# Kernel tuning notes

Measured on AMD Instinct MI355X. Metric: run time of the kernel, lower is better.

## Reference

```python
import jax, jax.numpy as jnp
import numpy as np
from itertools import combinations

H_RANK_MAX = 2
TP_RANK_MAX = 2
BASIS_RANK_MAX = 2
DIM = 3
N_NODES = 50000
N_EDGES = 400000
N_CHANNELS = 16
R_CUT = 10.0  # radial cutoff for Bessel RBF (assumed)


def find_combinations(a_max, b_max, s):
    if s > a_max + b_max or s < 0:
        return []
    return [(a, s - a) for a in range(max(0, s - b_max), min(a_max, s) + 1)]


def contraction_is_valid(n_in, n_out):
    # legs are removed in pairs (Kronecker-delta contractions)
    return (n_in >= n_out) and ((n_in - n_out) % 2 == 0)


def _matchings(legs):
    # all perfect matchings of an even-size list of leg indices
    if not legs:
        yield []
        return
    a = legs[0]
    for i in range(1, len(legs)):
        rest = legs[1:i] + legs[i + 1:]
        for m in _matchings(rest):
            yield [(a, legs[i])] + m


def contraction_specs(a, b, c_out):
    # all einsum strings contracting an [E,K,dim^a] x [E,K,dim^b] tensor product
    # (a+b legs total) down to c_out free Cartesian legs, pairing the rest.
    n = a + b
    specs = []
    for free in combinations(range(n), c_out):
        paired = [i for i in range(n) if i not in free]
        for m in _matchings(paired):
            lbl = {}
            it = iter('mnopqrstuvwxyz')
            for f in free:
                lbl[f] = next(it)
            for (i, j) in m:
                L = next(it)
                lbl[i] = L
                lbl[j] = L
            sa = ''.join(lbl[i] for i in range(a))
            sb = ''.join(lbl[i] for i in range(a, n))
            so = ''.join(lbl[f] for f in free)
            specs.append(f'ek{sa},ek{sb}->ek{so}')
    return specs


def e_rbf(r, n):
    # Bessel radial basis: n is [K,1], r is [E] -> [K,E]
    return jnp.sqrt(2.0 / R_CUT) * jnp.sin(n * jnp.pi * r / R_CUT) / r


def tensor_prod(r, order):
    # repeated outer product of unit vectors: order 0 -> [E], order k -> [E] + [DIM]*k
    out = jnp.ones(r.shape[0], dtype=r.dtype)
    for _ in range(order):
        out = jnp.einsum('e...,ed->e...d', out, r)
    return out


def setup_inputs() -> dict:
    key = jax.random.key(0)
    ks = jax.random.split(key, 7)
    h0 = jax.random.normal(ks[0], (N_NODES, N_CHANNELS), jnp.float32)
    h1 = jax.random.normal(ks[1], (N_NODES, N_CHANNELS, DIM), jnp.float32)
    h2 = jax.random.normal(ks[2], (N_NODES, N_CHANNELS, DIM, DIM), jnp.float32)
    pos = jax.random.normal(ks[3], (N_NODES, DIM), jnp.float32)
    channel_weights = jax.random.normal(ks[4], (H_RANK_MAX + 1, N_CHANNELS, N_CHANNELS), jnp.float32)
    src = jax.random.randint(ks[5], (N_EDGES,), 0, N_NODES, dtype=jnp.int32)
    off = jax.random.randint(ks[6], (N_EDGES,), 1, N_NODES, dtype=jnp.int32)
    dst = (src + off) % N_NODES  # no self-loops -> no zero distances
    edge_index = jnp.stack([src, dst])
    return {"h0": h0, "h1": h1, "h2": h2, "pos": pos,
            "channel_weights": channel_weights, "edge_index": edge_index}


def reference(h0, h1, h2, pos, channel_weights, edge_index):
    h = [h0, h1, h2]
    src, dst = edge_index[0], edge_index[1]
    rel = pos[src] - pos[dst]                       # [E,3]
    dists = jnp.linalg.norm(rel, axis=-1)           # [E]
    unit = rel / dists[:, None]
    hg = [g[dst] for g in h]                        # per-edge gathered features
    # NOTE: the original forward computes channel-mixed self.h with channel_weights
    # but the contraction loop uses the UNMIXED gathered h (h[split[0]]); replicated here,
    # so channel_weights does not affect the output (zero gradient).
    n_vals = jnp.arange(1, N_CHANNELS + 1, dtype=dists.dtype)[:, None]  # [K,1]
    radial = e_rbf(dists, n_vals).reshape(N_EDGES, N_CHANNELS)  # faithful reshape (not transpose), as in source
    r_raw = [tensor_prod(unit, o) for o in range(TP_RANK_MAX + 1)]
    r_w = [jnp.einsum('ek,e...->ek...', radial, t) for t in r_raw]  # [E,K]+[3]*b
    outs = [None] * (BASIS_RANK_MAX + 1)
    for n_ind in range(H_RANK_MAX + TP_RANK_MAX + 1):
        for (a, b) in find_combinations(H_RANK_MAX, TP_RANK_MAX, n_ind):
            for br in range(BASIS_RANK_MAX + 1):
                if contraction_is_valid(n_ind, br):
                    for spec in contraction_specs(a, b, br):
                        t = jnp.einsum(spec, hg[a], r_w[b])
                        outs[br] = t if outs[br] is None else outs[br] + t
    # sum over paths (done incrementally above == stack + 'i...->...'), scatter to nodes
    res = []
    for t in outs:
        if t is not None:
            res.append(jax.ops.segment_sum(t, src, num_segments=N_NODES))
    return tuple(res)
```

## Files before the change

kernel.cpp:

```cpp
#include <hip/hip_runtime.h>
#include <math.h>

#define N_NODES   50000
#define N_EDGES   400000
#define NCH       16
#define RCUT      10.0f

__global__ void geom_hist_kernel(const float* __restrict__ pos,
                                 const int* __restrict__ src,
                                 const int* __restrict__ dst,
                                 float* __restrict__ dists,
                                 int* __restrict__ cnt) {
    int e = blockIdx.x * blockDim.x + threadIdx.x;
    if (e >= N_EDGES) return;
    int s = src[e];
    int d = dst[e];
    float rx = pos[3 * s + 0] - pos[3 * d + 0];
    float ry = pos[3 * s + 1] - pos[3 * d + 1];
    float rz = pos[3 * s + 2] - pos[3 * d + 2];
    dists[e] = sqrtf(rx * rx + ry * ry + rz * rz);
    atomicAdd(&cnt[s], 1);
}

__global__ void scan_blocks_kernel(const int* __restrict__ cnt,
                                   int* __restrict__ incl,
                                   int* __restrict__ bsum) {
    __shared__ int sh[256];
    int t = threadIdx.x;
    int i = blockIdx.x * 256 + t;
    int v = (i < N_NODES) ? cnt[i] : 0;
    sh[t] = v;
    __syncthreads();
    for (int s = 1; s < 256; s <<= 1) {
        int x = 0;
        if (t >= s) x = sh[t - s];
        __syncthreads();
        if (t >= s) sh[t] += x;
        __syncthreads();
    }
    if (i < N_NODES) incl[i] = sh[t];
    if (t == 255) bsum[blockIdx.x] = sh[255];
}

__global__ void finalize_kernel(const int* __restrict__ cnt,
                                const int* __restrict__ incl,
                                const int* __restrict__ bsum,
                                int* __restrict__ offsets,
                                int* __restrict__ cursor) {
    __shared__ int sh[256];
    int t = threadIdx.x;
    int b = blockIdx.x;
    sh[t] = (t < b) ? bsum[t] : 0;
    __syncthreads();
    for (int s = 128; s > 0; s >>= 1) {
        if (t < s) sh[t] += sh[t + s];
        __syncthreads();
    }
    int base = sh[0];
    int i = b * 256 + t;
    if (i < N_NODES) {
        int off = incl[i] - cnt[i] + base;
        offsets[i] = off;
        cursor[i] = off;
    }
    if (b == 0 && t == 0) offsets[N_NODES] = N_EDGES;
}

__global__ void fill_kernel(const int* __restrict__ src,
                            const int* __restrict__ dst,
                            const float* __restrict__ pos,
                            int* __restrict__ cursor,
                            float4* __restrict__ edata,
                            int* __restrict__ csr) {
    int e = blockIdx.x * blockDim.x + threadIdx.x;
    if (e >= N_EDGES) return;
    int s = src[e];
    int d = dst[e];
    float rx = pos[3 * s + 0] - pos[3 * d + 0];
    float ry = pos[3 * s + 1] - pos[3 * d + 1];
    float rz = pos[3 * s + 2] - pos[3 * d + 2];
    float inv = 1.0f / sqrtf(rx * rx + ry * ry + rz * rz);
    int slot = atomicAdd(&cursor[s], 1);
    float4 ed;
    ed.x = rx * inv;
    ed.y = ry * inv;
    ed.z = rz * inv;
    ed.w = __int_as_float(d);
    edata[slot] = ed;
    csr[slot] = e;
}

__global__ void node_wave_kernel(const float* __restrict__ h0,
                                 const float* __restrict__ h1,
                                 const float* __restrict__ h2,
                                 const int* __restrict__ offsets,
                                 const float4* __restrict__ edata,
                                 const int* __restrict__ csr,
                                 const float* __restrict__ dists,
                                 float* __restrict__ out0,
                                 float* __restrict__ out1,
                                 float* __restrict__ out2) {
    int gid = blockIdx.x * blockDim.x + threadIdx.x;
    int node = gid >> 6;
    if (node >= N_NODES) return;
    int lane = threadIdx.x & 63;
    int k = lane & 15;
    int j = lane >> 4;
    int beg = offsets[node];
    int end = offsets[node + 1];

    float acc0 = 0.0f;
    float acc1[3] = {0.0f, 0.0f, 0.0f};
    float acc2[9] = {0.0f, 0.0f, 0.0f, 0.0f, 0.0f, 0.0f, 0.0f, 0.0f, 0.0f};

    int i = beg + j;
    float4 ed;
    int e = 0;
    if (i < end) {
        ed = edata[i];
        e = csr[i];
    }
    while (i < end) {
        int inext = i + 4;
        float4 edn = ed;
        int en = e;
        if (inext < end) {
            edn = edata[inext];
            en = csr[inext];
        }

        int d = __float_as_int(ed.w);

        unsigned f = (unsigned)e * NCH + (unsigned)k;
        unsigned n_idx = f / (unsigned)N_EDGES;
        unsigned e_idx = f - n_idx * (unsigned)N_EDGES;
        float r = dists[e_idx];
        float R = 0.44721359549995794f *
                  __sinf((float)(n_idx + 1) * 0.3141592653589793f * r) / r;

        float ux = ed.x, uy = ed.y, uz = ed.z;
        float u[3] = {ux, uy, uz};

        float A0 = h0[d * NCH + k];
        const float* a1p = h1 + ((size_t)d * NCH + k) * 3;
        float A1[3] = {a1p[0], a1p[1], a1p[2]};
        const float* a2p = h2 + ((size_t)d * NCH + k) * 9;
        float A2[9];
#pragma unroll
        for (int q2 = 0; q2 < 9; ++q2) A2[q2] = a2p[q2];

        float d1 = A1[0] * ux + A1[1] * uy + A1[2] * uz;
        float tA = A2[0] + A2[4] + A2[8];
        float v0 = A2[0] * ux + A2[1] * uy + A2[2] * uz;
        float v1 = A2[3] * ux + A2[4] * uy + A2[5] * uz;
        float v2 = A2[6] * ux + A2[7] * uy + A2[8] * uz;
        float w0 = A2[0] * ux + A2[3] * uy + A2[6] * uz;
        float w1 = A2[1] * ux + A2[4] * uy + A2[7] * uz;
        float w2 = A2[2] * ux + A2[5] * uy + A2[8] * uz;
        float q = ux * v0 + uy * v1 + uz * v2;

        acc0 += R * (2.0f * A0 + d1 + 2.0f * tA + 2.0f * q);

        float svw[3] = {v0 + w0, v1 + w1, v2 + w2};
        float a0t = A0 + tA;
#pragma unroll
        for (int m = 0; m < 3; ++m) {
            acc1[m] += R * (A0 * u[m] + 2.0f * A1[m] + 2.0f * d1 * u[m]
                            + svw[m] + tA * u[m]);
#pragma unroll
            for (int nn = 0; nn < 3; ++nn) {
                acc2[3 * m + nn] += R * (a0t * u[m] * u[nn] + A1[m] * u[nn]
                                         + 2.0f * A2[3 * m + nn]
                                         + 2.0f * svw[m] * u[nn]);
            }
        }

        ed = edn;
        e = en;
        i = inext;
    }

    acc0 += __shfl_xor(acc0, 16, 64);
    acc0 += __shfl_xor(acc0, 32, 64);
#pragma unroll
    for (int m = 0; m < 3; ++m) {
        acc1[m] += __shfl_xor(acc1[m], 16, 64);
        acc1[m] += __shfl_xor(acc1[m], 32, 64);
    }
#pragma unroll
    for (int m = 0; m < 9; ++m) {
        acc2[m] += __shfl_xor(acc2[m], 16, 64);
        acc2[m] += __shfl_xor(acc2[m], 32, 64);
    }

    if (j == 0) {
        int t = node * NCH + k;
        out0[t] = acc0;
        float* o1p = out1 + (size_t)t * 3;
#pragma unroll
        for (int m = 0; m < 3; ++m) o1p[m] = acc1[m];
        float* o2p = out2 + (size_t)t * 9;
#pragma unroll
        for (int m = 0; m < 9; ++m) o2p[m] = acc2[m];
    }
}

extern "C" void kernel_launch(void* const* d_in, const int* in_sizes, int n_in,
                              void* d_out, int out_size, void* d_ws, size_t ws_size,
                              hipStream_t stream) {
    const float* h0  = (const float*)d_in[0];
    const float* h1  = (const float*)d_in[1];
    const float* h2  = (const float*)d_in[2];
    const float* pos = (const float*)d_in[3];
    const int* edge_index = (const int*)d_in[5];
    const int* src = edge_index;
    const int* dst = edge_index + N_EDGES;

    float* out = (float*)d_out;
    float* out0 = out;
    float* out1 = out + (size_t)N_NODES * NCH;
    float* out2 = out + (size_t)N_NODES * NCH * 4;

    float4* edata  = (float4*)d_ws;
    float*  dists  = (float*)(edata + N_EDGES);
    int* csr       = (int*)(dists + N_EDGES);
    int* cnt       = csr + N_EDGES;
    int* incl      = cnt + N_NODES;
    int* bsum      = incl + N_NODES;
    int* offsets   = bsum + 256;
    int* cursor    = offsets + N_NODES + 1;

    const int NB_EDGES = (N_EDGES + 255) / 256;
    const int NB_NODES = (N_NODES + 255) / 256;

    hipMemsetAsync(cnt, 0, N_NODES * sizeof(int), stream);
    geom_hist_kernel<<<NB_EDGES, 256, 0, stream>>>(pos, src, dst, dists, cnt);
    scan_blocks_kernel<<<NB_NODES, 256, 0, stream>>>(cnt, incl, bsum);
    finalize_kernel<<<NB_NODES, 256, 0, stream>>>(cnt, incl, bsum, offsets, cursor);
    fill_kernel<<<NB_EDGES, 256, 0, stream>>>(src, dst, pos, cursor, edata, csr);

    const int TOTAL = N_NODES * 64;
    node_wave_kernel<<<(TOTAL + 255) / 256, 256, 0, stream>>>(
        h0, h1, h2, offsets, edata, csr, dists, out0, out1, out2);
}
```

Before: 203.8 us.

## Fuse CSR build and node accumulation into one cooperative persistent kernel

Replaces the memset plus five separate launches with a single cooperative kernel that uses grid-wide syncs between the histogram, scan, finalize, fill and accumulation phases. Per-edge slot ranks are recorded during the histogram, and counters are striped eight ways by block to reduce atomic contention, so the fill pass no longer needs atomics. The accumulation phase becomes a persistent grid-stride loop over nodes. In exchange it adds grid.sync overhead, limits the grid to occupancy-bounded residency, and keeps a multi-kernel fallback path if the cooperative launch fails.

```diff
diff --git a/kernel.cpp b/kernel.cpp
--- a/kernel.cpp
+++ b/kernel.cpp
@@ -1,111 +1,27 @@
 #include <hip/hip_runtime.h>
+#include <hip/hip_cooperative_groups.h>
 #include <math.h>
+
+namespace cg = cooperative_groups;
 
 #define N_NODES   50000
 #define N_EDGES   400000
 #define NCH       16
-#define RCUT      10.0f
-
-__global__ void geom_hist_kernel(const float* __restrict__ pos,
-                                 const int* __restrict__ src,
-                                 const int* __restrict__ dst,
-                                 float* __restrict__ dists,
-                                 int* __restrict__ cnt) {
-    int e = blockIdx.x * blockDim.x + threadIdx.x;
-    if (e >= N_EDGES) return;
-    int s = src[e];
-    int d = dst[e];
-    float rx = pos[3 * s + 0] - pos[3 * d + 0];
-    float ry = pos[3 * s + 1] - pos[3 * d + 1];
-    float rz = pos[3 * s + 2] - pos[3 * d + 2];
-    dists[e] = sqrtf(rx * rx + ry * ry + rz * rz);
-    atomicAdd(&cnt[s], 1);
-}
-
-__global__ void scan_blocks_kernel(const int* __restrict__ cnt,
-                                   int* __restrict__ incl,
-                                   int* __restrict__ bsum) {
-    __shared__ int sh[256];
-    int t = threadIdx.x;
-    int i = blockIdx.x * 256 + t;
-    int v = (i < N_NODES) ? cnt[i] : 0;
-    sh[t] = v;
-    __syncthreads();
-    for (int s = 1; s < 256; s <<= 1) {
-        int x = 0;
-        if (t >= s) x = sh[t - s];
-        __syncthreads();
-        if (t >= s) sh[t] += x;
-        __syncthreads();
-    }
-    if (i < N_NODES) incl[i] = sh[t];
-    if (t == 255) bsum[blockIdx.x] = sh[255];
-}
-
-__global__ void finalize_kernel(const int* __restrict__ cnt,
-                                const int* __restrict__ incl,
-                                const int* __restrict__ bsum,
-                                int* __restrict__ offsets,
-                                int* __restrict__ cursor) {
-    __shared__ int sh[256];
-    int t = threadIdx.x;
-    int b = blockIdx.x;
-    sh[t] = (t < b) ? bsum[t] : 0;
-    __syncthreads();
-    for (int s = 128; s > 0; s >>= 1) {
-        if (t < s) sh[t] += sh[t + s];
-        __syncthreads();
-    }
-    int base = sh[0];
-    int i = b * 256 + t;
-    if (i < N_NODES) {
-        int off = incl[i] - cnt[i] + base;
-        offsets[i] = off;
-        cursor[i] = off;
-    }
-    if (b == 0 && t == 0) offsets[N_NODES] = N_EDGES;
-}
-
-__global__ void fill_kernel(const int* __restrict__ src,
-                            const int* __restrict__ dst,
-                            const float* __restrict__ pos,
-                            int* __restrict__ cursor,
-                            float4* __restrict__ edata,
-                            int* __restrict__ csr) {
-    int e = blockIdx.x * blockDim.x + threadIdx.x;
-    if (e >= N_EDGES) return;
-    int s = src[e];
-    int d = dst[e];
-    float rx = pos[3 * s + 0] - pos[3 * d + 0];
-    float ry = pos[3 * s + 1] - pos[3 * d + 1];
-    float rz = pos[3 * s + 2] - pos[3 * d + 2];
-    float inv = 1.0f / sqrtf(rx * rx + ry * ry + rz * rz);
-    int slot = atomicAdd(&cursor[s], 1);
-    float4 ed;
-    ed.x = rx * inv;
-    ed.y = ry * inv;
-    ed.z = rz * inv;
-    ed.w = __int_as_float(d);
-    edata[slot] = ed;
-    csr[slot] = e;
-}
-
-__global__ void node_wave_kernel(const float* __restrict__ h0,
-                                 const float* __restrict__ h1,
-                                 const float* __restrict__ h2,
-                                 const int* __restrict__ offsets,
-                                 const float4* __restrict__ edata,
-                                 const int* __restrict__ csr,
-                                 const float* __restrict__ dists,
-                                 float* __restrict__ out0,
-                                 float* __restrict__ out1,
-                                 float* __restrict__ out2) {
-    int gid = blockIdx.x * blockDim.x + threadIdx.x;
-    int node = gid >> 6;
-    if (node >= N_NODES) return;
-    int lane = threadIdx.x & 63;
-    int k = lane & 15;
-    int j = lane >> 4;
+#define NSTRIPE   8
+#define BLOCKS_MAX 1024
+#define TPB       256
+#define NBN       ((N_NODES + TPB - 1) / TPB)
+#define NB_EDGES  ((N_EDGES + TPB - 1) / TPB)
+
+
+__device__ __forceinline__ void accum_node(
+    int node, int k, int j,
+    const float* __restrict__ h0, const float* __restrict__ h1,
+    const float* __restrict__ h2, const int* __restrict__ offsets,
+    const float4* __restrict__ edata, const int* __restrict__ csr,
+    const float* __restrict__ dists,
+    float* __restrict__ out0, float* __restrict__ out1, float* __restrict__ out2)
+{
     int beg = offsets[node];
     int end = offsets[node + 1];
 
@@ -116,18 +32,12 @@
     int i = beg + j;
     float4 ed;
     int e = 0;
-    if (i < end) {
-        ed = edata[i];
-        e = csr[i];
-    }
+    if (i < end) { ed = edata[i]; e = csr[i]; }
     while (i < end) {
         int inext = i + 4;
         float4 edn = ed;
         int en = e;
-        if (inext < end) {
-            edn = edata[inext];
-            en = csr[inext];
-        }
+        if (inext < end) { edn = edata[inext]; en = csr[inext]; }
 
         int d = __float_as_int(ed.w);
 
@@ -204,6 +114,244 @@
         for (int m = 0; m < 9; ++m) o2p[m] = acc2[m];
     }
 }
+
+
+__global__ __launch_bounds__(TPB, 4)
+void fused_kernel(const float* __restrict__ h0,
+                  const float* __restrict__ h1,
+                  const float* __restrict__ h2,
+                  const float* __restrict__ pos,
+                  const int* __restrict__ src,
+                  const int* __restrict__ dst,
+                  int* __restrict__ cnt8,
+                  int* __restrict__ rankArr,
+                  float* __restrict__ dists,
+                  int* __restrict__ incl,
+                  int* __restrict__ bsum,
+                  int* __restrict__ offsets,
+                  int* __restrict__ copyBase,
+                  float4* __restrict__ edata,
+                  int* __restrict__ csr,
+                  float* __restrict__ out0,
+                  float* __restrict__ out1,
+                  float* __restrict__ out2)
+{
+    cg::grid_group grid = cg::this_grid();
+    __shared__ int sh[TPB];
+
+    const int tid  = threadIdx.x;
+    const int gtid = blockIdx.x * TPB + tid;
+    const int GT   = gridDim.x * TPB;
+    const int stripe = blockIdx.x & (NSTRIPE - 1);
+
+    for (int i = gtid; i < NSTRIPE * N_NODES; i += GT) cnt8[i] = 0;
+    grid.sync();
+
+    for (int e = gtid; e < N_EDGES; e += GT) {
+        int s = src[e];
+        int d = dst[e];
+        float rx = pos[3 * s + 0] - pos[3 * d + 0];
+        float ry = pos[3 * s + 1] - pos[3 * d + 1];
+        float rz = pos[3 * s + 2] - pos[3 * d + 2];
+        dists[e] = sqrtf(rx * rx + ry * ry + rz * rz);
+        rankArr[e] = atomicAdd(&cnt8[stripe * N_NODES + s], 1);
+    }
+    grid.sync();
+
+    if (blockIdx.x < NBN) {
+        int i = blockIdx.x * TPB + tid;
+        int tot = 0;
+        if (i < N_NODES) {
+#pragma unroll
+            for (int c = 0; c < NSTRIPE; ++c) tot += cnt8[c * N_NODES + i];
+        }
+        sh[tid] = tot;
+        __syncthreads();
+        for (int s = 1; s < TPB; s <<= 1) {
+            int x = 0;
+            if (tid >= s) x = sh[tid - s];
+            __syncthreads();
+            if (tid >= s) sh[tid] += x;
+            __syncthreads();
+        }
+        if (i < N_NODES) incl[i] = sh[tid];
+        if (tid == TPB - 1) bsum[blockIdx.x] = sh[TPB - 1];
+    }
+    grid.sync();
+
+    if (blockIdx.x < NBN) {
+        int b = blockIdx.x;
+        sh[tid] = (tid < b) ? bsum[tid] : 0;
+        __syncthreads();
+        for (int s = 128; s > 0; s >>= 1) {
+            if (tid < s) sh[tid] += sh[tid + s];
+            __syncthreads();
+        }
+        int base = sh[0];
+        int i = b * TPB + tid;
+        if (i < N_NODES) {
+            int cv[NSTRIPE];
+            int tot = 0;
+#pragma unroll
+            for (int c = 0; c < NSTRIPE; ++c) { cv[c] = cnt8[c * N_NODES + i]; tot += cv[c]; }
+            int off = base + incl[i] - tot;
+            offsets[i] = off;
+            int run = off;
+#pragma unroll
+            for (int c = 0; c < NSTRIPE; ++c) { copyBase[c * N_NODES + i] = run; run += cv[c]; }
+        }
+        if (b == 0 && tid == 0) offsets[N_NODES] = N_EDGES;
+    }
+    grid.sync();
+
+    for (int e = gtid; e < N_EDGES; e += GT) {
+        int s = src[e];
+        int d = dst[e];
+        float rx = pos[3 * s + 0] - pos[3 * d + 0];
+        float ry = pos[3 * s + 1] - pos[3 * d + 1];
+        float rz = pos[3 * s + 2] - pos[3 * d + 2];
+        float inv = 1.0f / dists[e];
+        int slot = copyBase[stripe * N_NODES + s] + rankArr[e];
+        float4 ed;
+        ed.x = rx * inv;
+        ed.y = ry * inv;
+        ed.z = rz * inv;
+        ed.w = __int_as_float(d);
+        edata[slot] = ed;
+        csr[slot] = e;
+    }
+    grid.sync();
+
+    const int lane = tid & 63;
+    const int k = lane & 15;
+    const int j = lane >> 4;
+    const int wid = gtid >> 6;
+    const int NW = GT >> 6;
+
+    for (int node = wid; node < N_NODES; node += NW) {
+        accum_node(node, k, j, h0, h1, h2, offsets, edata, csr, dists,
+                   out0, out1, out2);
+    }
+}
+
+
+__global__ void fb_geom_hist(const float* __restrict__ pos,
+                             const int* __restrict__ src,
+                             const int* __restrict__ dst,
+                             float* __restrict__ dists,
+                             int* __restrict__ cnt8,
+                             int* __restrict__ rankArr) {
+    int e = blockIdx.x * TPB + threadIdx.x;
+    if (e >= N_EDGES) return;
+    int stripe = blockIdx.x & (NSTRIPE - 1);
+    int s = src[e];
+    int d = dst[e];
+    float rx = pos[3 * s + 0] - pos[3 * d + 0];
+    float ry = pos[3 * s + 1] - pos[3 * d + 1];
+    float rz = pos[3 * s + 2] - pos[3 * d + 2];
+    dists[e] = sqrtf(rx * rx + ry * ry + rz * rz);
+    rankArr[e] = atomicAdd(&cnt8[stripe * N_NODES + s], 1);
+}
+
+__global__ void fb_scan(const int* __restrict__ cnt8,
+                        int* __restrict__ incl,
+                        int* __restrict__ bsum) {
+    __shared__ int sh[TPB];
+    int tid = threadIdx.x;
+    int i = blockIdx.x * TPB + tid;
+    int tot = 0;
+    if (i < N_NODES) {
+#pragma unroll
+        for (int c = 0; c < NSTRIPE; ++c) tot += cnt8[c * N_NODES + i];
+    }
+    sh[tid] = tot;
+    __syncthreads();
+    for (int s = 1; s < TPB; s <<= 1) {
+        int x = 0;
+        if (tid >= s) x = sh[tid - s];
+        __syncthreads();
+        if (tid >= s) sh[tid] += x;
+        __syncthreads();
+    }
+    if (i < N_NODES) incl[i] = sh[tid];
+    if (tid == TPB - 1) bsum[blockIdx.x] = sh[TPB - 1];
+}
+
+__global__ void fb_final(const int* __restrict__ cnt8,
+                         const int* __restrict__ incl,
+                         const int* __restrict__ bsum,
+                         int* __restrict__ offsets,
+                         int* __restrict__ copyBase) {
+    __shared__ int sh[TPB];
+    int tid = threadIdx.x;
+    int b = blockIdx.x;
+    sh[tid] = (tid < b) ? bsum[tid] : 0;
+    __syncthreads();
+    for (int s = 128; s > 0; s >>= 1) {
+        if (tid < s) sh[tid] += sh[tid + s];
+        __syncthreads();
+    }
+    int base = sh[0];
+    int i = b * TPB + tid;
+    if (i < N_NODES) {
+        int cv[NSTRIPE];
+        int tot = 0;
+#pragma unroll
+        for (int c = 0; c < NSTRIPE; ++c) { cv[c] = cnt8[c * N_NODES + i]; tot += cv[c]; }
+        int off = base + incl[i] - tot;
+        offsets[i] = off;
+        int run = off;
+#pragma unroll
+        for (int c = 0; c < NSTRIPE; ++c) { copyBase[c * N_NODES + i] = run; run += cv[c]; }
+    }
+    if (b == 0 && tid == 0) offsets[N_NODES] = N_EDGES;
+}
+
+__global__ void fb_fill(const int* __restrict__ src,
+                        const int* __restrict__ dst,
+                        const float* __restrict__ pos,
+                        const float* __restrict__ dists,
+                        const int* __restrict__ copyBase,
+                        const int* __restrict__ rankArr,
+                        float4* __restrict__ edata,
+                        int* __restrict__ csr) {
+    int e = blockIdx.x * TPB + threadIdx.x;
+    if (e >= N_EDGES) return;
+    int stripe = blockIdx.x & (NSTRIPE - 1);
+    int s = src[e];
+    int d = dst[e];
+    float rx = pos[3 * s + 0] - pos[3 * d + 0];
+    float ry = pos[3 * s + 1] - pos[3 * d + 1];
+    float rz = pos[3 * s + 2] - pos[3 * d + 2];
+    float inv = 1.0f / dists[e];
+    int slot = copyBase[stripe * N_NODES + s] + rankArr[e];
+    float4 ed;
+    ed.x = rx * inv;
+    ed.y = ry * inv;
+    ed.z = rz * inv;
+    ed.w = __int_as_float(d);
+    edata[slot] = ed;
+    csr[slot] = e;
+}
+
+__global__ void fb_main(const float* __restrict__ h0,
+                        const float* __restrict__ h1,
+                        const float* __restrict__ h2,
+                        const int* __restrict__ offsets,
+                        const float4* __restrict__ edata,
+                        const int* __restrict__ csr,
+                        const float* __restrict__ dists,
+                        float* __restrict__ out0,
+                        float* __restrict__ out1,
+                        float* __restrict__ out2) {
+    int gid = blockIdx.x * TPB + threadIdx.x;
+    int node = gid >> 6;
+    if (node >= N_NODES) return;
+    int lane = threadIdx.x & 63;
+    accum_node(node, lane & 15, lane >> 4, h0, h1, h2, offsets, edata, csr,
+               dists, out0, out1, out2);
+}
+
 
 extern "C" void kernel_launch(void* const* d_in, const int* in_sizes, int n_in,
                               void* d_out, int out_size, void* d_ws, size_t ws_size,
@@ -221,25 +369,45 @@
     float* out1 = out + (size_t)N_NODES * NCH;
     float* out2 = out + (size_t)N_NODES * NCH * 4;
 
-    float4* edata  = (float4*)d_ws;
-    float*  dists  = (float*)(edata + N_EDGES);
-    int* csr       = (int*)(dists + N_EDGES);
-    int* cnt       = csr + N_EDGES;
-    int* incl      = cnt + N_NODES;
-    int* bsum      = incl + N_NODES;
-    int* offsets   = bsum + 256;
-    int* cursor    = offsets + N_NODES + 1;
-
-    const int NB_EDGES = (N_EDGES + 255) / 256;
-    const int NB_NODES = (N_NODES + 255) / 256;
-
-    hipMemsetAsync(cnt, 0, N_NODES * sizeof(int), stream);
-    geom_hist_kernel<<<NB_EDGES, 256, 0, stream>>>(pos, src, dst, dists, cnt);
-    scan_blocks_kernel<<<NB_NODES, 256, 0, stream>>>(cnt, incl, bsum);
-    finalize_kernel<<<NB_NODES, 256, 0, stream>>>(cnt, incl, bsum, offsets, cursor);
-    fill_kernel<<<NB_EDGES, 256, 0, stream>>>(src, dst, pos, cursor, edata, csr);
-
-    const int TOTAL = N_NODES * 64;
-    node_wave_kernel<<<(TOTAL + 255) / 256, 256, 0, stream>>>(
-        h0, h1, h2, offsets, edata, csr, dists, out0, out1, out2);
-}
+    float4* edata   = (float4*)d_ws;
+    float*  dists   = (float*)(edata + N_EDGES);
+    int* cnt8       = (int*)(dists + N_EDGES);
+    int* rankArr    = cnt8 + NSTRIPE * N_NODES;
+    int* incl       = rankArr + N_EDGES;
+    int* bsum       = incl + N_NODES;
+    int* offsets    = bsum + 256;
+    int* copyBase   = offsets + N_NODES + 1;
+    int* csr        = copyBase + NSTRIPE * N_NODES;
+
+    int occ = 0;
+    hipError_t qerr = hipOccupancyMaxActiveBlocksPerMultiprocessor(
+        &occ, fused_kernel, TPB, 0);
+    int blocks = (qerr == hipSuccess) ? occ * 256 : 0;
+    if (blocks > BLOCKS_MAX) blocks = BLOCKS_MAX;
+
+    bool coop_done = false;
+    if (blocks >= 256) {
+        void* args[] = {
+            (void*)&h0, (void*)&h1, (void*)&h2, (void*)&pos,
+            (void*)&src, (void*)&dst,
+            (void*)&cnt8, (void*)&rankArr, (void*)&dists,
+            (void*)&incl, (void*)&bsum, (void*)&offsets, (void*)&copyBase,
+            (void*)&edata, (void*)&csr,
+            (void*)&out0, (void*)&out1, (void*)&out2
+        };
+        hipError_t lerr = hipLaunchCooperativeKernel((const void*)fused_kernel,
+                                                     dim3(blocks), dim3(TPB),
+                                                     args, 0, stream);
+        coop_done = (lerr == hipSuccess);
+    }
+
+    if (!coop_done) {
+        hipMemsetAsync(cnt8, 0, NSTRIPE * N_NODES * sizeof(int), stream);
+        fb_geom_hist<<<NB_EDGES, TPB, 0, stream>>>(pos, src, dst, dists, cnt8, rankArr);
+        fb_scan<<<NBN, TPB, 0, stream>>>(cnt8, incl, bsum);
+        fb_final<<<NBN, TPB, 0, stream>>>(cnt8, incl, bsum, offsets, copyBase);
+        fb_fill<<<NB_EDGES, TPB, 0, stream>>>(src, dst, pos, dists, copyBase, rankArr, edata, csr);
+        fb_main<<<(N_NODES * 64 + TPB - 1) / TPB, TPB, 0, stream>>>(
+            h0, h1, h2, offsets, edata, csr, dists, out0, out1, out2);
+    }
+}
```

Result: slower. 602.0 us (+195.5%).

## Stripe degree histogram, drop fill atomics, and prefetch neighbor features

Applied to the files above, without the earlier changes.

The degree histogram now uses 8 block-striped counters, and each edge records its rank from that atomic. The fill pass then computes CSR slots from per-stripe bases without a second round of atomics, and reuses the stored distance instead of recomputing a sqrt. The node kernel loads the next edge's neighbor h0/h1/h2 features one iteration ahead to hide gather latency. The cost is a larger workspace, an extra rank array read and written, and more live registers in the main kernel.

```diff
diff --git a/kernel.cpp b/kernel.cpp
--- a/kernel.cpp
+++ b/kernel.cpp
@@ -4,83 +4,101 @@
 #define N_NODES   50000
 #define N_EDGES   400000
 #define NCH       16
-#define RCUT      10.0f
+#define NSTRIPE   8
+#define TPB       256
+#define NBN       ((N_NODES + TPB - 1) / TPB)
+#define NB_EDGES  ((N_EDGES + TPB - 1) / TPB)
 
 __global__ void geom_hist_kernel(const float* __restrict__ pos,
                                  const int* __restrict__ src,
                                  const int* __restrict__ dst,
                                  float* __restrict__ dists,
-                                 int* __restrict__ cnt) {
-    int e = blockIdx.x * blockDim.x + threadIdx.x;
+                                 int* __restrict__ cnt8,
+                                 int* __restrict__ rankArr) {
+    int e = blockIdx.x * TPB + threadIdx.x;
     if (e >= N_EDGES) return;
+    int stripe = blockIdx.x & (NSTRIPE - 1);
     int s = src[e];
     int d = dst[e];
     float rx = pos[3 * s + 0] - pos[3 * d + 0];
     float ry = pos[3 * s + 1] - pos[3 * d + 1];
     float rz = pos[3 * s + 2] - pos[3 * d + 2];
     dists[e] = sqrtf(rx * rx + ry * ry + rz * rz);
-    atomicAdd(&cnt[s], 1);
-}
-
-__global__ void scan_blocks_kernel(const int* __restrict__ cnt,
-                                   int* __restrict__ incl,
-                                   int* __restrict__ bsum) {
-    __shared__ int sh[256];
-    int t = threadIdx.x;
-    int i = blockIdx.x * 256 + t;
-    int v = (i < N_NODES) ? cnt[i] : 0;
-    sh[t] = v;
+    rankArr[e] = atomicAdd(&cnt8[stripe * N_NODES + s], 1);
+}
+
+__global__ void scan_kernel(const int* __restrict__ cnt8,
+                            int* __restrict__ incl,
+                            int* __restrict__ bsum) {
+    __shared__ int sh[TPB];
+    int tid = threadIdx.x;
+    int i = blockIdx.x * TPB + tid;
+    int tot = 0;
+    if (i < N_NODES) {
+#pragma unroll
+        for (int c = 0; c < NSTRIPE; ++c) tot += cnt8[c * N_NODES + i];
+    }
+    sh[tid] = tot;
     __syncthreads();
-    for (int s = 1; s < 256; s <<= 1) {
+    for (int s = 1; s < TPB; s <<= 1) {
         int x = 0;
-        if (t >= s) x = sh[t - s];
+        if (tid >= s) x = sh[tid - s];
         __syncthreads();
-        if (t >= s) sh[t] += x;
+        if (tid >= s) sh[tid] += x;
         __syncthreads();
     }
-    if (i < N_NODES) incl[i] = sh[t];
-    if (t == 255) bsum[blockIdx.x] = sh[255];
-}
-
-__global__ void finalize_kernel(const int* __restrict__ cnt,
-                                const int* __restrict__ incl,
-                                const int* __restrict__ bsum,
-                                int* __restrict__ offsets,
-                                int* __restrict__ cursor) {
-    __shared__ int sh[256];
-    int t = threadIdx.x;
+    if (i < N_NODES) incl[i] = sh[tid];
+    if (tid == TPB - 1) bsum[blockIdx.x] = sh[TPB - 1];
+}
+
+__global__ void final_kernel(const int* __restrict__ cnt8,
+                             const int* __restrict__ incl,
+                             const int* __restrict__ bsum,
+                             int* __restrict__ offsets,
+                             int* __restrict__ copyBase) {
+    __shared__ int sh[TPB];
+    int tid = threadIdx.x;
     int b = blockIdx.x;
-    sh[t] = (t < b) ? bsum[t] : 0;
+    sh[tid] = (tid < b) ? bsum[tid] : 0;
     __syncthreads();
     for (int s = 128; s > 0; s >>= 1) {
-        if (t < s) sh[t] += sh[t + s];
+        if (tid < s) sh[tid] += sh[tid + s];
         __syncthreads();
     }
     int base = sh[0];
-    int i = b * 256 + t;
+    int i = b * TPB + tid;
     if (i < N_NODES) {
-        int off = incl[i] - cnt[i] + base;
+        int cv[NSTRIPE];
+        int tot = 0;
+#pragma unroll
+        for (int c = 0; c < NSTRIPE; ++c) { cv[c] = cnt8[c * N_NODES + i]; tot += cv[c]; }
+        int off = base + incl[i] - tot;
         offsets[i] = off;
-        cursor[i] = off;
-    }
-    if (b == 0 && t == 0) offsets[N_NODES] = N_EDGES;
+        int run = off;
+#pragma unroll
+        for (int c = 0; c < NSTRIPE; ++c) { copyBase[c * N_NODES + i] = run; run += cv[c]; }
+    }
+    if (b == 0 && tid == 0) offsets[N_NODES] = N_EDGES;
 }
 
 __global__ void fill_kernel(const int* __restrict__ src,
                             const int* __restrict__ dst,
                             const float* __restrict__ pos,
-                            int* __restrict__ cursor,
+                            const float* __restrict__ dists,
+                            const int* __restrict__ copyBase,
+                            const int* __restrict__ rankArr,
                             float4* __restrict__ edata,
                             int* __restrict__ csr) {
-    int e = blockIdx.x * blockDim.x + threadIdx.x;
+    int e = blockIdx.x * TPB + threadIdx.x;
     if (e >= N_EDGES) return;
+    int stripe = blockIdx.x & (NSTRIPE - 1);
     int s = src[e];
     int d = dst[e];
     float rx = pos[3 * s + 0] - pos[3 * d + 0];
     float ry = pos[3 * s + 1] - pos[3 * d + 1];
     float rz = pos[3 * s + 2] - pos[3 * d + 2];
-    float inv = 1.0f / sqrtf(rx * rx + ry * ry + rz * rz);
-    int slot = atomicAdd(&cursor[s], 1);
+    float inv = 1.0f / dists[e];
+    int slot = copyBase[stripe * N_NODES + s] + rankArr[e];
     float4 ed;
     ed.x = rx * inv;
     ed.y = ry * inv;
@@ -100,7 +118,7 @@
                                  float* __restrict__ out0,
                                  float* __restrict__ out1,
                                  float* __restrict__ out2) {
-    int gid = blockIdx.x * blockDim.x + threadIdx.x;
+    int gid = blockIdx.x * TPB + threadIdx.x;
     int node = gid >> 6;
     if (node >= N_NODES) return;
     int lane = threadIdx.x & 63;
@@ -114,63 +132,78 @@
     float acc2[9] = {0.0f, 0.0f, 0.0f, 0.0f, 0.0f, 0.0f, 0.0f, 0.0f, 0.0f};
 
     int i = beg + j;
-    float4 ed;
+    float4 ed = make_float4(0.f, 0.f, 0.f, 0.f);
     int e = 0;
+    float A0 = 0.f, A1[3] = {0.f, 0.f, 0.f};
+    float A2[9] = {0.f, 0.f, 0.f, 0.f, 0.f, 0.f, 0.f, 0.f, 0.f};
     if (i < end) {
         ed = edata[i];
         e = csr[i];
-    }
+        int d = __float_as_int(ed.w);
+        A0 = h0[d * NCH + k];
+        const float* a1p = h1 + ((size_t)d * NCH + k) * 3;
+#pragma unroll
+        for (int m = 0; m < 3; ++m) A1[m] = a1p[m];
+        const float* a2p = h2 + ((size_t)d * NCH + k) * 9;
+#pragma unroll
+        for (int m = 0; m < 9; ++m) A2[m] = a2p[m];
+    }
+
     while (i < end) {
         int inext = i + 4;
         float4 edn = ed;
         int en = e;
+        if (inext < end) { edn = edata[inext]; en = csr[inext]; }
+
+        float B0 = A0;
+        float B1[3] = {A1[0], A1[1], A1[2]};
+        float B2[9];
+#pragma unroll
+        for (int m = 0; m < 9; ++m) B2[m] = A2[m];
+        float ux = ed.x, uy = ed.y, uz = ed.z;
+        int ecur = e;
+
         if (inext < end) {
-            edn = edata[inext];
-            en = csr[inext];
+            int dn = __float_as_int(edn.w);
+            A0 = h0[dn * NCH + k];
+            const float* a1p = h1 + ((size_t)dn * NCH + k) * 3;
+#pragma unroll
+            for (int m = 0; m < 3; ++m) A1[m] = a1p[m];
+            const float* a2p = h2 + ((size_t)dn * NCH + k) * 9;
+#pragma unroll
+            for (int m = 0; m < 9; ++m) A2[m] = a2p[m];
         }
 
-        int d = __float_as_int(ed.w);
-
-        unsigned f = (unsigned)e * NCH + (unsigned)k;
+        unsigned f = (unsigned)ecur * NCH + (unsigned)k;
         unsigned n_idx = f / (unsigned)N_EDGES;
         unsigned e_idx = f - n_idx * (unsigned)N_EDGES;
         float r = dists[e_idx];
         float R = 0.44721359549995794f *
                   __sinf((float)(n_idx + 1) * 0.3141592653589793f * r) / r;
 
-        float ux = ed.x, uy = ed.y, uz = ed.z;
         float u[3] = {ux, uy, uz};
-
-        float A0 = h0[d * NCH + k];
-        const float* a1p = h1 + ((size_t)d * NCH + k) * 3;
-        float A1[3] = {a1p[0], a1p[1], a1p[2]};
-        const float* a2p = h2 + ((size_t)d * NCH + k) * 9;
-        float A2[9];
-#pragma unroll
-        for (int q2 = 0; q2 < 9; ++q2) A2[q2] = a2p[q2];
-
-        float d1 = A1[0] * ux + A1[1] * uy + A1[2] * uz;
-        float tA = A2[0] + A2[4] + A2[8];
-        float v0 = A2[0] * ux + A2[1] * uy + A2[2] * uz;
-        float v1 = A2[3] * ux + A2[4] * uy + A2[5] * uz;
-        float v2 = A2[6] * ux + A2[7] * uy + A2[8] * uz;
-        float w0 = A2[0] * ux + A2[3] * uy + A2[6] * uz;
-        float w1 = A2[1] * ux + A2[4] * uy + A2[7] * uz;
-        float w2 = A2[2] * ux + A2[5] * uy + A2[8] * uz;
+        float d1 = B1[0] * ux + B1[1] * uy + B1[2] * uz;
+        float tA = B2[0] + B2[4] + B2[8];
+        float v0 = B2[0] * ux + B2[1] * uy + B2[2] * uz;
+        float v1 = B2[3] * ux + B2[4] * uy + B2[5] * uz;
+        float v2 = B2[6] * ux + B2[7] * uy + B2[8] * uz;
+        float w0 = B2[0] * ux + B2[3] * uy + B2[6] * uz;
+        float w1 = B2[1] * ux + B2[4] * uy + B2[7] * uz;
+        float w2 = B2[2] * ux + B2[5] * uy + B2[8] * uz;
         float q = ux * v0 + uy * v1 + uz * v2;
 
-        acc0 += R * (2.0f * A0 + d1 + 2.0f * tA + 2.0f * q);
+        acc0 += R * (2.0f * B0 + d1 + 2.0f * tA + 2.0f * q);
 
         float svw[3] = {v0 + w0, v1 + w1, v2 + w2};
-        float a0t = A0 + tA;
+        float a0t = B0 + tA;
 #pragma unroll
         for (int m = 0; m < 3; ++m) {
-            acc1[m] += R * (A0 * u[m] + 2.0f * A1[m] + 2.0f * d1 * u[m]
+            acc1[m] += R * (B0 * u[m] + 2.0f * B1[m] + 2.0f * d1 * u[m]
                             + svw[m] + tA * u[m]);
 #pragma unroll
             for (int nn = 0; nn < 3; ++nn) {
-                acc2[3 * m + nn] += R * (a0t * u[m] * u[nn] + A1[m] * u[nn]
-                                         + 2.0f * A2[3 * m + nn]
+                acc2[3 * m + nn] += R * (a0t * u[m] * u[nn] + B1[m] * u[nn]
+                                         + 2.0f * B2[3 * m + nn]
                                          + 2.0f * svw[m] * u[nn]);
             }
         }
@@ -221,25 +254,21 @@
     float* out1 = out + (size_t)N_NODES * NCH;
     float* out2 = out + (size_t)N_NODES * NCH * 4;
 
-    float4* edata  = (float4*)d_ws;
-    float*  dists  = (float*)(edata + N_EDGES);
-    int* csr       = (int*)(dists + N_EDGES);
-    int* cnt       = csr + N_EDGES;
-    int* incl      = cnt + N_NODES;
-    int* bsum      = incl + N_NODES;
-    int* offsets   = bsum + 256;
-    int* cursor    = offsets + N_NODES + 1;
-
-    const int NB_EDGES = (N_EDGES + 255) / 256;
-    const int NB_NODES = (N_NODES + 255) / 256;
-
-    hipMemsetAsync(cnt, 0, N_NODES * sizeof(int), stream);
-    geom_hist_kernel<<<NB_EDGES, 256, 0, stream>>>(pos, src, dst, dists, cnt);
-    scan_blocks_kernel<<<NB_NODES, 256, 0, stream>>>(cnt, incl, bsum);
-    finalize_kernel<<<NB_NODES, 256, 0, stream>>>(cnt, incl, bsum, offsets, cursor);
-    fill_kernel<<<NB_EDGES, 256, 0, stream>>>(src, dst, pos, cursor, edata, csr);
-
-    const int TOTAL = N_NODES * 64;
-    node_wave_kernel<<<(TOTAL + 255) / 256, 256, 0, stream>>>(
+    float4* edata   = (float4*)d_ws;
+    float*  dists   = (float*)(edata + N_EDGES);
+    int* cnt8       = (int*)(dists + N_EDGES);
+    int* rankArr    = cnt8 + NSTRIPE * N_NODES;
+    int* incl       = rankArr + N_EDGES;
+    int* bsum       = incl + N_NODES;
+    int* offsets    = bsum + 256;
+    int* copyBase   = offsets + N_NODES + 1;
+    int* csr        = copyBase + NSTRIPE * N_NODES;
+
+    hipMemsetAsync(cnt8, 0, NSTRIPE * N_NODES * sizeof(int), stream);
+    geom_hist_kernel<<<NB_EDGES, TPB, 0, stream>>>(pos, src, dst, dists, cnt8, rankArr);
+    scan_kernel<<<NBN, TPB, 0, stream>>>(cnt8, incl, bsum);
+    final_kernel<<<NBN, TPB, 0, stream>>>(cnt8, incl, bsum, offsets, copyBase);
+    fill_kernel<<<NB_EDGES, TPB, 0, stream>>>(src, dst, pos, dists, copyBase, rankArr, edata, csr);
+    node_wave_kernel<<<(N_NODES * 64 + TPB - 1) / TPB, TPB, 0, stream>>>(
         h0, h1, h2, offsets, edata, csr, dists, out0, out1, out2);
 }
```

Result: faster. 198.9 us (-2.4%).
